# Kernel tuning notes

Hardware: AMD Instinct MI355X
Metric: run time of the kernel (lower is better)

The kernel has to match this reference:

```python
import jax, jax.numpy as jnp
import numpy as np

B, S, D, E, K = 4, 4096, 1024, 8, 2
H = 2 * D  # expert hidden dim


def setup_inputs() -> dict:
    key = jax.random.key(0)
    ks = jax.random.split(key, 7)
    scale = 0.02
    return {
        "x": jax.random.normal(ks[0], (B, S, D), dtype=jnp.float32),
        "router_w": jax.random.normal(ks[1], (D, E), dtype=jnp.float32) * scale,
        "router_b": jnp.zeros((E,), dtype=jnp.float32),
        "w1": jax.random.normal(ks[2], (E, D, H), dtype=jnp.float32) * scale,
        "b1": jnp.zeros((E, H), dtype=jnp.float32),
        "w2": jax.random.normal(ks[3], (E, H, D), dtype=jnp.float32) * scale,
        "b2": jnp.zeros((E, D), dtype=jnp.float32),
    }


def reference(x, router_w, router_b, w1, b1, w2, b2):
    # Router: softmax over experts, then top-k and renormalize
    logits = jnp.einsum("bsd,de->bse", x, router_w) + router_b
    probs = jax.nn.softmax(logits, axis=-1)
    top_p, top_i = jax.lax.top_k(probs, K)             # [B,S,K]
    top_p = top_p / jnp.sum(top_p, axis=-1, keepdims=True)

    out = jnp.zeros_like(x)
    for e in range(E):
        # gate weight for expert e per token (0 if not routed)
        gate = jnp.sum(top_p * (top_i == e), axis=-1)  # [B,S]
        h = jax.nn.relu(jnp.einsum("bsd,dh->bsh", x, w1[e]) + b1[e])
        y = jnp.einsum("bsh,hd->bsd", h, w2[e]) + b2[e]
        out = out + y * gate[..., None]
    return out
```

## Files before the change

kernel.cpp:

```cpp
#include <hip/hip_runtime.h>
#include <cstdio>
#include <cstdint>

#define N_TOK 16384
#define DIM   1024
#define NEXP  8
#define HID   2048
#define BK    64

typedef __attribute__((ext_vector_type(8))) short bf16x8;
typedef __attribute__((ext_vector_type(4))) float f32x4;

__device__ inline ushort f2bf(float f) {
  uint32_t u = __float_as_uint(f);
  uint32_t r = (u + 0x7fffu + ((u >> 16) & 1u)) >> 16;
  return (ushort)r;
}
__device__ inline float bf2f(ushort u) { return __uint_as_float(((uint32_t)u) << 16); }

__device__ __forceinline__ void gload_lds16(const void* g, void* l) {
  __builtin_amdgcn_global_load_lds((const __attribute__((address_space(1))) void*)g,
                                   (__attribute__((address_space(3))) void*)l, 16, 0, 0);
}

#define WAITV0() asm volatile("s_waitcnt vmcnt(0)" ::: "memory")
#define PBAR()  do { __builtin_amdgcn_s_barrier(); __builtin_amdgcn_sched_barrier(0); } while (0)

__global__ __launch_bounds__(256) void router_kernel(
    const float* __restrict__ x, const float* __restrict__ rw,
    const float* __restrict__ rb, int* __restrict__ blkcnt,
    int* __restrict__ tok_e, float* __restrict__ tok_g,
    ushort* __restrict__ xb) {
  __shared__ float wT[NEXP][DIM];
  __shared__ int hist[NEXP];
  if (threadIdx.x < NEXP) hist[threadIdx.x] = 0;
  for (int i = threadIdx.x; i < NEXP * DIM; i += 256) {
    int d = i >> 3, e = i & 7;
    wT[e][d] = rw[i];
  }
  __syncthreads();
  int wave = threadIdx.x >> 6, lane = threadIdx.x & 63;
  int t0 = blockIdx.x * 16 + wave * 4;
#pragma unroll
  for (int it = 0; it < 4; ++it) {
    int t = t0 + it;
    const float* xr = x + (size_t)t * DIM;
    float acc[NEXP];
#pragma unroll
    for (int e = 0; e < NEXP; ++e) acc[e] = 0.f;
#pragma unroll
    for (int j = 0; j < DIM / 64; ++j) {
      int d = lane + j * 64;
      float xv = xr[d];
#pragma unroll
      for (int e = 0; e < NEXP; ++e) acc[e] += xv * wT[e][d];
    }
    float lg[NEXP];
#pragma unroll
    for (int e = 0; e < NEXP; ++e) {
      float v = acc[e];
      for (int o = 32; o > 0; o >>= 1) v += __shfl_xor(v, o);
      lg[e] = v + rb[e];
    }
    int i0 = 0; float m0 = lg[0];
#pragma unroll
    for (int e = 1; e < NEXP; ++e) if (lg[e] > m0) { m0 = lg[e]; i0 = e; }
    int i1 = -1; float m1 = -3.4e38f;
#pragma unroll
    for (int e = 0; e < NEXP; ++e) if (e != i0 && lg[e] > m1) { m1 = lg[e]; i1 = e; }
    float g0 = 1.f / (1.f + expf(m1 - m0));
    float g1 = 1.f - g0;
    if (lane == 0) {
      tok_e[2 * t] = i0; tok_e[2 * t + 1] = i1;
      tok_g[2 * t] = g0; tok_g[2 * t + 1] = g1;
      atomicAdd(&hist[i0], 1); atomicAdd(&hist[i1], 1);
    }
  }
  {
    const float* xs = x + (size_t)blockIdx.x * 16 * DIM;
    ushort* xd = xb + (size_t)blockIdx.x * 16 * DIM;
    for (int i = threadIdx.x; i < 16 * DIM / 4; i += 256) {
      float4 v = *(const float4*)(xs + i * 4);
      ushort4 u = { f2bf(v.x), f2bf(v.y), f2bf(v.z), f2bf(v.w) };
      *(ushort4*)(xd + i * 4) = u;
    }
  }
  __syncthreads();
  if (threadIdx.x < NEXP) blkcnt[blockIdx.x * NEXP + threadIdx.x] = hist[threadIdx.x];
}

__global__ __launch_bounds__(512) void scan_kernel(const int* __restrict__ blkcnt,
                                                   int* __restrict__ blkbase,
                                                   int* __restrict__ offs) {
  __shared__ int s[64][8];
  __shared__ int chunkoff[64][8];
  __shared__ int offsh[8];
  int tid = threadIdx.x;
  int e = tid & 7, chunk = tid >> 3;
  int b0 = chunk * 16;
  int csum = 0;
#pragma unroll
  for (int b = 0; b < 16; ++b) csum += blkcnt[(b0 + b) * 8 + e];
  s[chunk][e] = csum;
  __syncthreads();
  int wave = tid >> 6, lane = tid & 63;
  int v = s[lane][wave];
  for (int o = 1; o < 64; o <<= 1) {
    int u = __shfl_up(v, o);
    if (lane >= o) v += u;
  }
  if (lane == 63) offsh[wave] = v;
  chunkoff[lane][wave] = v - s[lane][wave];
  __syncthreads();
  if (tid < 9) {
    int oe = 0;
    for (int j = 0; j < tid && j < 8; ++j) oe += offsh[j];
    offs[tid] = oe;
  }
  int oe2 = 0;
#pragma unroll
  for (int j = 0; j < 8; ++j) oe2 += (j < e) ? offsh[j] : 0;
  int base = oe2 + chunkoff[chunk][e];
  for (int b = 0; b < 16; ++b) {
    int idx = (b0 + b) * 8 + e;
    int c = blkcnt[idx];
    blkbase[idx] = base;
    base += c;
  }
}

__global__ __launch_bounds__(64) void gather_kernel(
    const int* __restrict__ tok_e, const float* __restrict__ tok_g,
    const int* __restrict__ blkbase, int* __restrict__ slot_token,
    float* __restrict__ slot_gate) {
  __shared__ int lcnt[NEXP];
  int tid = threadIdx.x, blk = blockIdx.x;
  if (tid < NEXP) lcnt[tid] = blkbase[blk * NEXP + tid];
  __syncthreads();
  if (tid < 32) {
    int t = blk * 16 + (tid >> 1);
    int k = tid & 1;
    int e = tok_e[2 * t + k];
    int s = atomicAdd(&lcnt[e], 1);
    slot_token[s] = t | (k << 16);
    slot_gate[s] = tok_g[2 * t + k];
  }
}

template <int R, int C>
__global__ __launch_bounds__(256) void transpose_cvt(const float* __restrict__ src,
                                                     ushort* __restrict__ dst) {
  __shared__ float tile[64][65];
  int e = blockIdx.z;
  const float* s = src + (size_t)e * R * C;
  ushort* d = dst + (size_t)e * R * C;
  int r0 = blockIdx.y * 64, c0 = blockIdx.x * 64;
#pragma unroll
  for (int i = 0; i < 16; ++i) {
    int idx = i * 256 + threadIdx.x;
    int r = idx >> 6, c = idx & 63;
    tile[r][c] = s[(size_t)(r0 + r) * C + c0 + c];
  }
  __syncthreads();
#pragma unroll
  for (int i = 0; i < 16; ++i) {
    int idx = i * 256 + threadIdx.x;
    int orow = idx >> 6, oc = idx & 63;
    d[(size_t)(c0 + orow) * R + r0 + oc] = f2bf(tile[oc][orow]);
  }
}


__global__ __launch_bounds__(512, 1) void gemm1_kernel(
    const ushort* __restrict__ xb, const ushort* __restrict__ w1T,
    const float* __restrict__ b1, const int* __restrict__ offs,
    const int* __restrict__ slot_token, ushort* __restrict__ h) {
  int flat = blockIdx.x;
  int swz = (flat & 7) * 512 + (flat >> 3);
  int e = swz >> 9;
  int rem = swz & 511;
  int mt = rem >> 3;
  int nt = rem & 7;
  int off = offs[e];
  int cn = offs[e + 1] - off;
  if (mt * 256 >= cn) return;

  __shared__ __align__(16) ushort AB[2 * 2 * 16384];
  __shared__ int toks[256];
  int tid = threadIdx.x;
  if (tid < 256) {
    int r = mt * 256 + tid;
    toks[tid] = slot_token[off + (r < cn ? r : 0)] & 0xffff;
  }
  __syncthreads();
  int wave = tid >> 6, lane = tid & 63;
  int wm = (wave >> 2) * 128, wn = (wave & 3) * 64;

  const ushort* Bsrc = w1T + (size_t)e * HID * DIM + (size_t)(nt * 256) * DIM;
  int colsw = (((lane & 7) ^ (lane >> 3))) * 8;
  const ushort* agp[4];
  const ushort* bgp[4];
  int ldso[4];
#pragma unroll
  for (int g = 0; g < 4; ++g) {
    int row = g * 64 + wave * 8 + (lane >> 3);
    agp[g] = xb + (size_t)toks[row] * DIM + colsw;
    bgp[g] = Bsrc + (size_t)row * DIM + colsw;
    ldso[g] = (g * 64 + wave * 8) * BK;
  }
  f32x4 acc[8][4];
#pragma unroll
  for (int i = 0; i < 8; ++i)
#pragma unroll
    for (int j = 0; j < 4; ++j) acc[i][j] = (f32x4){0.f, 0.f, 0.f, 0.f};

  int rowl = lane & 15;
  int ko0 = ((((lane >> 4) + 0)) ^ (lane & 7)) * 16 + rowl * 128;
  int ko1 = ((((lane >> 4) + 4)) ^ (lane & 7)) * 16 + rowl * 128;

  auto stage = [&](int buf) {
    ushort* lb = &AB[buf * 32768];
#pragma unroll
    for (int g = 0; g < 4; ++g) {
      gload_lds16(agp[g], lb + ldso[g]);
      gload_lds16(bgp[g], lb + 16384 + ldso[g]);
      agp[g] += BK; bgp[g] += BK;
    }
  };
  auto compute = [&](int buf) {
    const char* base = (const char*)AB + buf * 65536;
    const char* bbase = base + 32768;
    bf16x8 a[8], b[4];
#pragma unroll
    for (int mi = 0; mi < 8; ++mi) a[mi] = *(const bf16x8*)(base + (wm + mi * 16) * 128 + ko0);
#pragma unroll
    for (int ni = 0; ni < 4; ++ni) b[ni] = *(const bf16x8*)(bbase + (wn + ni * 16) * 128 + ko0);
#pragma unroll
    for (int mi = 0; mi < 8; ++mi)
#pragma unroll
      for (int ni = 0; ni < 4; ++ni)
        acc[mi][ni] = __builtin_amdgcn_mfma_f32_16x16x32_bf16(a[mi], b[ni], acc[mi][ni], 0, 0, 0);
#pragma unroll
    for (int mi = 0; mi < 8; ++mi) a[mi] = *(const bf16x8*)(base + (wm + mi * 16) * 128 + ko1);
#pragma unroll
    for (int ni = 0; ni < 4; ++ni) b[ni] = *(const bf16x8*)(bbase + (wn + ni * 16) * 128 + ko1);
#pragma unroll
    for (int mi = 0; mi < 8; ++mi)
#pragma unroll
      for (int ni = 0; ni < 4; ++ni)
        acc[mi][ni] = __builtin_amdgcn_mfma_f32_16x16x32_bf16(a[mi], b[ni], acc[mi][ni], 0, 0, 0);
  };

  const int NT = DIM / BK;
  stage(0); WAITV0(); PBAR();
  for (int kt = 0; kt < NT - 2; kt += 2) {
    stage(1); compute(0); WAITV0(); PBAR();
    stage(0); compute(1); WAITV0(); PBAR();
  }
  stage(1); compute(0); WAITV0(); PBAR();
  compute(1);

  __syncthreads();
  char* Cb = (char*)AB;
  int ln = lane & 15, lg4 = (lane >> 4) * 4;
#pragma unroll
  for (int ni = 0; ni < 4; ++ni) {
    int coll = wn + ni * 16 + ln;
    float bias = b1[(size_t)e * HID + nt * 256 + coll];
#pragma unroll
    for (int mi = 0; mi < 8; ++mi) {
#pragma unroll
      for (int rg = 0; rg < 4; ++rg) {
        int row = wm + mi * 16 + lg4 + rg;
        float v = fmaxf(acc[mi][ni][rg] + bias, 0.f);
        int slot = (coll >> 3) ^ (row & 7);
        *(ushort*)(Cb + row * 512 + slot * 16 + (coll & 7) * 2) = f2bf(v);
      }
    }
  }
  __syncthreads();
#pragma unroll
  for (int rr = 0; rr < 16; ++rr) {
    int row = rr * 16 + (tid >> 5);
    int scol = tid & 31;
    int4 v = *(const int4*)(Cb + row * 512 + ((scol ^ (row & 7)) << 4));
    int r = mt * 256 + row;
    if (r < cn)
      *(int4*)(h + (size_t)(off + r) * HID + nt * 256 + scol * 8) = v;
  }
}

__global__ __launch_bounds__(512, 1) void gemm2_kernel(
    const ushort* __restrict__ h, const ushort* __restrict__ w2T,
    const float* __restrict__ b2, const int* __restrict__ offs,
    const int* __restrict__ slot_token, const float* __restrict__ slot_gate,
    ushort* __restrict__ y) {
  int flat = blockIdx.x;
  int swz = (flat & 7) * 256 + (flat >> 3);
  int e = swz >> 8;
  int rem = swz & 255;
  int mt = rem >> 2;
  int nt = rem & 3;
  int off = offs[e];
  int cn = offs[e + 1] - off;
  if (mt * 256 >= cn) return;

  __shared__ __align__(16) ushort AB[2 * 2 * 16384];
  __shared__ int yrows[256];
  __shared__ float gts[256];
  int tid = threadIdx.x;
  if (tid < 256) {
    int r = mt * 256 + tid;
    int s = off + (r < cn ? r : 0);
    int tk = slot_token[s];
    yrows[tid] = ((tk & 0xffff) << 1) | (tk >> 16);
    gts[tid] = slot_gate[s];
  }
  __syncthreads();
  int wave = tid >> 6, lane = tid & 63;
  int wm = (wave >> 2) * 128, wn = (wave & 3) * 64;

  const ushort* Bsrc = w2T + (size_t)e * DIM * HID + (size_t)(nt * 256) * HID;
  int colsw = (((lane & 7) ^ (lane >> 3))) * 8;
  const ushort* agp[4];
  const ushort* bgp[4];
  int ldso[4];
#pragma unroll
  for (int g = 0; g < 4; ++g) {
    int row = g * 64 + wave * 8 + (lane >> 3);
    int rr = mt * 256 + row; rr = rr < cn ? rr : 0;
    agp[g] = h + (size_t)(off + rr) * HID + colsw;
    bgp[g] = Bsrc + (size_t)row * HID + colsw;
    ldso[g] = (g * 64 + wave * 8) * BK;
  }
  f32x4 acc[8][4];
#pragma unroll
  for (int i = 0; i < 8; ++i)
#pragma unroll
    for (int j = 0; j < 4; ++j) acc[i][j] = (f32x4){0.f, 0.f, 0.f, 0.f};

  int rowl = lane & 15;
  int ko0 = ((((lane >> 4) + 0)) ^ (lane & 7)) * 16 + rowl * 128;
  int ko1 = ((((lane >> 4) + 4)) ^ (lane & 7)) * 16 + rowl * 128;

  auto stage = [&](int buf) {
    ushort* lb = &AB[buf * 32768];
#pragma unroll
    for (int g = 0; g < 4; ++g) {
      gload_lds16(agp[g], lb + ldso[g]);
      gload_lds16(bgp[g], lb + 16384 + ldso[g]);
      agp[g] += BK; bgp[g] += BK;
    }
  };
  auto compute = [&](int buf) {
    const char* base = (const char*)AB + buf * 65536;
    const char* bbase = base + 32768;
    bf16x8 a[8], b[4];
#pragma unroll
    for (int mi = 0; mi < 8; ++mi) a[mi] = *(const bf16x8*)(base + (wm + mi * 16) * 128 + ko0);
#pragma unroll
    for (int ni = 0; ni < 4; ++ni) b[ni] = *(const bf16x8*)(bbase + (wn + ni * 16) * 128 + ko0);
#pragma unroll
    for (int mi = 0; mi < 8; ++mi)
#pragma unroll
      for (int ni = 0; ni < 4; ++ni)
        acc[mi][ni] = __builtin_amdgcn_mfma_f32_16x16x32_bf16(a[mi], b[ni], acc[mi][ni], 0, 0, 0);
#pragma unroll
    for (int mi = 0; mi < 8; ++mi) a[mi] = *(const bf16x8*)(base + (wm + mi * 16) * 128 + ko1);
#pragma unroll
    for (int ni = 0; ni < 4; ++ni) b[ni] = *(const bf16x8*)(bbase + (wn + ni * 16) * 128 + ko1);
#pragma unroll
    for (int mi = 0; mi < 8; ++mi)
#pragma unroll
      for (int ni = 0; ni < 4; ++ni)
        acc[mi][ni] = __builtin_amdgcn_mfma_f32_16x16x32_bf16(a[mi], b[ni], acc[mi][ni], 0, 0, 0);
  };

  const int NT = HID / BK;
  stage(0); WAITV0(); PBAR();
  for (int kt = 0; kt < NT - 2; kt += 2) {
    stage(1); compute(0); WAITV0(); PBAR();
    stage(0); compute(1); WAITV0(); PBAR();
  }
  stage(1); compute(0); WAITV0(); PBAR();
  compute(1);

  __syncthreads();
  char* Cb = (char*)AB;
  int ln = lane & 15, lg4 = (lane >> 4) * 4;
#pragma unroll
  for (int ni = 0; ni < 4; ++ni) {
    int coll = wn + ni * 16 + ln;
    float bias = b2[(size_t)e * DIM + nt * 256 + coll];
#pragma unroll
    for (int mi = 0; mi < 8; ++mi) {
#pragma unroll
      for (int rg = 0; rg < 4; ++rg) {
        int row = wm + mi * 16 + lg4 + rg;
        float v = gts[row] * (acc[mi][ni][rg] + bias);
        int slot = (coll >> 3) ^ (row & 7);
        *(ushort*)(Cb + row * 512 + slot * 16 + (coll & 7) * 2) = f2bf(v);
      }
    }
  }
  __syncthreads();
#pragma unroll
  for (int rr = 0; rr < 16; ++rr) {
    int row = rr * 16 + (tid >> 5);
    int scol = tid & 31;
    int4 v = *(const int4*)(Cb + row * 512 + ((scol ^ (row & 7)) << 4));
    int r = mt * 256 + row;
    if (r < cn)
      *(int4*)(y + (size_t)yrows[row] * DIM + nt * 256 + scol * 8) = v;
  }
}

__global__ __launch_bounds__(256) void combine_kernel(float* __restrict__ out) {
  int t = blockIdx.x;
  int d = threadIdx.x;
  const ushort* y = (const ushort*)out;
  ushort4 a = *(const ushort4*)(y + (size_t)(2 * t) * DIM + 4 * d);
  ushort4 b = *(const ushort4*)(y + (size_t)(2 * t + 1) * DIM + 4 * d);
  float4 r;
  r.x = bf2f(a.x) + bf2f(b.x);
  r.y = bf2f(a.y) + bf2f(b.y);
  r.z = bf2f(a.z) + bf2f(b.z);
  r.w = bf2f(a.w) + bf2f(b.w);
  __syncthreads();
  *(float4*)(out + (size_t)t * DIM + 4 * d) = r;
}

extern "C" void kernel_launch(void* const* d_in, const int* in_sizes, int n_in,
                              void* d_out, int out_size, void* d_ws, size_t ws_size,
                              hipStream_t stream) {
  const float* x  = (const float*)d_in[0];
  const float* rw = (const float*)d_in[1];
  const float* rb = (const float*)d_in[2];
  const float* w1 = (const float*)d_in[3];
  const float* b1 = (const float*)d_in[4];
  const float* w2 = (const float*)d_in[5];
  const float* b2 = (const float*)d_in[6];
  float* out = (float*)d_out;
  char* ws = (char*)d_ws;

  const size_t o_ctrl = 0;
  const size_t o_toke = 256;
  const size_t o_tokg = o_toke + 131072;
  const size_t o_stok = o_tokg + 131072;
  const size_t o_sgat = o_stok + 131072;
  const size_t o_xb   = o_sgat + 131072;
  const size_t o_w1T  = o_xb + (size_t)N_TOK * DIM * 2;
  const size_t o_h    = o_w1T + (size_t)NEXP * HID * DIM * 2;
  const size_t required = o_h + (size_t)N_TOK * 2 * HID * 2;
  if (ws_size < required) {
    fprintf(stderr, "kernel_launch: ws too small: have %zu need %zu\n", ws_size, required);
    return;
  }
  int* offs       = (int*)(ws + o_ctrl);
  int* tok_e      = (int*)(ws + o_toke);
  float* tok_g    = (float*)(ws + o_tokg);
  int* slot_token = (int*)(ws + o_stok);
  float* slot_gate= (float*)(ws + o_sgat);
  ushort* xb      = (ushort*)(ws + o_xb);
  ushort* w2T     = (ushort*)(ws + o_xb);
  ushort* w1T     = (ushort*)(ws + o_w1T);
  ushort* hbuf    = (ushort*)(ws + o_h);
  int* blkcnt     = (int*)(ws + o_h);
  int* blkbase    = blkcnt + 1024 * NEXP;

  hipMemsetAsync(d_out, 0, (size_t)out_size * 4, stream);
  hipMemsetAsync(ws + o_ctrl, 0, 64, stream);

  router_kernel<<<N_TOK / 16, 256, 0, stream>>>(x, rw, rb, blkcnt, tok_e, tok_g, xb);
  scan_kernel<<<1, 512, 0, stream>>>(blkcnt, blkbase, offs);
  gather_kernel<<<N_TOK / 16, 64, 0, stream>>>(tok_e, tok_g, blkbase, slot_token, slot_gate);

  transpose_cvt<DIM, HID><<<dim3(HID / 64, DIM / 64, NEXP), 256, 0, stream>>>(w1, w1T);

  gemm1_kernel<<<8 * 64 * NEXP, 512, 0, stream>>>(xb, w1T, b1, offs, slot_token, hbuf);

  transpose_cvt<HID, DIM><<<dim3(DIM / 64, HID / 64, NEXP), 256, 0, stream>>>(w2, w2T);

  gemm2_kernel<<<4 * 64 * NEXP, 512, 0, stream>>>(hbuf, w2T, b2, offs, slot_token, slot_gate,
                                                  (ushort*)d_out);
  combine_kernel<<<N_TOK, 256, 0, stream>>>(out);
}
```

Measured before the change: 454.2 us.

## Deepen GEMM pipelines to four LDS stages with BK=32 and drop memsets

Both expert GEMM kernels switch from a double-buffered BK=64 loop that waits for all loads each step to a four-buffer BK=32 ring. Three stages are kept in flight, and partial vmcnt waits let global-to-LDS loads overlap MFMA work instead of draining the queue at every step. The LDS swizzle and the per-lane load mapping are reworked for the 64-byte rows. Separately, the two hipMemsetAsync calls on the output and control area are removed. That saves launches but is only correct if nothing depends on the zeroing, which is a risk for the offset/control counters.

Result: faster. 431.5 us (-5.0%).

```diff
diff --git a/kernel.cpp b/kernel.cpp
--- a/kernel.cpp
+++ b/kernel.cpp
@@ -6,7 +6,7 @@
 #define DIM   1024
 #define NEXP  8
 #define HID   2048
-#define BK    64
+#define BK    32
 
 typedef __attribute__((ext_vector_type(8))) short bf16x8;
 typedef __attribute__((ext_vector_type(4))) float f32x4;
@@ -23,7 +23,7 @@
                                    (__attribute__((address_space(3))) void*)l, 16, 0, 0);
 }
 
-#define WAITV0() asm volatile("s_waitcnt vmcnt(0)" ::: "memory")
+#define WAITV(N) asm volatile("s_waitcnt vmcnt(" #N ")" ::: "memory")
 #define PBAR()  do { __builtin_amdgcn_s_barrier(); __builtin_amdgcn_sched_barrier(0); } while (0)
 
 __global__ __launch_bounds__(256) void router_kernel(
@@ -185,7 +185,7 @@
   int cn = offs[e + 1] - off;
   if (mt * 256 >= cn) return;
 
-  __shared__ __align__(16) ushort AB[2 * 2 * 16384];
+  __shared__ __align__(16) ushort AB[4 * 16384];
   __shared__ int toks[256];
   int tid = threadIdx.x;
   if (tid < 256) {
@@ -197,53 +197,41 @@
   int wm = (wave >> 2) * 128, wn = (wave & 3) * 64;
 
   const ushort* Bsrc = w1T + (size_t)e * HID * DIM + (size_t)(nt * 256) * DIM;
-  int colsw = (((lane & 7) ^ (lane >> 3))) * 8;
-  const ushort* agp[4];
-  const ushort* bgp[4];
-  int ldso[4];
-#pragma unroll
-  for (int g = 0; g < 4; ++g) {
-    int row = g * 64 + wave * 8 + (lane >> 3);
-    agp[g] = xb + (size_t)toks[row] * DIM + colsw;
-    bgp[g] = Bsrc + (size_t)row * DIM + colsw;
-    ldso[g] = (g * 64 + wave * 8) * BK;
-  }
+  int colsw = ((lane & 3) ^ ((lane >> 3) & 3)) * 8;
+  int r0 = wave * 16 + (lane >> 2);
+  const ushort* ag0 = xb + (size_t)toks[r0] * DIM + colsw;
+  const ushort* ag1 = xb + (size_t)toks[128 + r0] * DIM + colsw;
+  const ushort* bg0 = Bsrc + (size_t)r0 * DIM + colsw;
+  const ushort* bg1 = Bsrc + (size_t)(128 + r0) * DIM + colsw;
+  int ldsA0 = (wave * 16) * BK;
+  int ldsA1 = (128 + wave * 16) * BK;
+  int ldsB0 = 8192 + ldsA0;
+  int ldsB1 = 8192 + ldsA1;
+
   f32x4 acc[8][4];
 #pragma unroll
   for (int i = 0; i < 8; ++i)
 #pragma unroll
     for (int j = 0; j < 4; ++j) acc[i][j] = (f32x4){0.f, 0.f, 0.f, 0.f};
 
-  int rowl = lane & 15;
-  int ko0 = ((((lane >> 4) + 0)) ^ (lane & 7)) * 16 + rowl * 128;
-  int ko1 = ((((lane >> 4) + 4)) ^ (lane & 7)) * 16 + rowl * 128;
+  int rdo = (lane & 15) * 64 + ((((lane >> 4) & 3) << 4) ^ ((((lane & 15) >> 1) & 3) << 4));
 
   auto stage = [&](int buf) {
-    ushort* lb = &AB[buf * 32768];
-#pragma unroll
-    for (int g = 0; g < 4; ++g) {
-      gload_lds16(agp[g], lb + ldso[g]);
-      gload_lds16(bgp[g], lb + 16384 + ldso[g]);
-      agp[g] += BK; bgp[g] += BK;
-    }
+    ushort* lb = &AB[buf * 16384];
+    gload_lds16(ag0, lb + ldsA0); ag0 += BK;
+    gload_lds16(ag1, lb + ldsA1); ag1 += BK;
+    gload_lds16(bg0, lb + ldsB0); bg0 += BK;
+    gload_lds16(bg1, lb + ldsB1); bg1 += BK;
   };
   auto compute = [&](int buf) {
-    const char* base = (const char*)AB + buf * 65536;
-    const char* bbase = base + 32768;
+    const char* base = (const char*)AB + (size_t)buf * 32768;
     bf16x8 a[8], b[4];
 #pragma unroll
-    for (int mi = 0; mi < 8; ++mi) a[mi] = *(const bf16x8*)(base + (wm + mi * 16) * 128 + ko0);
-#pragma unroll
-    for (int ni = 0; ni < 4; ++ni) b[ni] = *(const bf16x8*)(bbase + (wn + ni * 16) * 128 + ko0);
-#pragma unroll
     for (int mi = 0; mi < 8; ++mi)
-#pragma unroll
-      for (int ni = 0; ni < 4; ++ni)
-        acc[mi][ni] = __builtin_amdgcn_mfma_f32_16x16x32_bf16(a[mi], b[ni], acc[mi][ni], 0, 0, 0);
-#pragma unroll
-    for (int mi = 0; mi < 8; ++mi) a[mi] = *(const bf16x8*)(base + (wm + mi * 16) * 128 + ko1);
-#pragma unroll
-    for (int ni = 0; ni < 4; ++ni) b[ni] = *(const bf16x8*)(bbase + (wn + ni * 16) * 128 + ko1);
+      a[mi] = *(const bf16x8*)(base + (wm + mi * 16) * 64 + rdo);
+#pragma unroll
+    for (int ni = 0; ni < 4; ++ni)
+      b[ni] = *(const bf16x8*)(base + 16384 + (wn + ni * 16) * 64 + rdo);
 #pragma unroll
     for (int mi = 0; mi < 8; ++mi)
 #pragma unroll
@@ -251,14 +239,18 @@
         acc[mi][ni] = __builtin_amdgcn_mfma_f32_16x16x32_bf16(a[mi], b[ni], acc[mi][ni], 0, 0, 0);
   };
 
-  const int NT = DIM / BK;
-  stage(0); WAITV0(); PBAR();
-  for (int kt = 0; kt < NT - 2; kt += 2) {
-    stage(1); compute(0); WAITV0(); PBAR();
-    stage(0); compute(1); WAITV0(); PBAR();
-  }
-  stage(1); compute(0); WAITV0(); PBAR();
-  compute(1);
+  const int T = DIM / BK;
+  stage(0); stage(1); stage(2);
+  for (int t4 = 0; t4 < T - 4; t4 += 4) {
+    WAITV(8); PBAR(); stage(3); compute(0);
+    WAITV(8); PBAR(); stage(0); compute(1);
+    WAITV(8); PBAR(); stage(1); compute(2);
+    WAITV(8); PBAR(); stage(2); compute(3);
+  }
+  WAITV(8); PBAR(); stage(3); compute(0);
+  WAITV(8); PBAR(); compute(1);
+  WAITV(4); PBAR(); compute(2);
+  WAITV(0); PBAR(); compute(3);
 
   __syncthreads();
   char* Cb = (char*)AB;
@@ -305,7 +297,7 @@
   int cn = offs[e + 1] - off;
   if (mt * 256 >= cn) return;
 
-  __shared__ __align__(16) ushort AB[2 * 2 * 16384];
+  __shared__ __align__(16) ushort AB[4 * 16384];
   __shared__ int yrows[256];
   __shared__ float gts[256];
   int tid = threadIdx.x;
@@ -321,54 +313,43 @@
   int wm = (wave >> 2) * 128, wn = (wave & 3) * 64;
 
   const ushort* Bsrc = w2T + (size_t)e * DIM * HID + (size_t)(nt * 256) * HID;
-  int colsw = (((lane & 7) ^ (lane >> 3))) * 8;
-  const ushort* agp[4];
-  const ushort* bgp[4];
-  int ldso[4];
-#pragma unroll
-  for (int g = 0; g < 4; ++g) {
-    int row = g * 64 + wave * 8 + (lane >> 3);
-    int rr = mt * 256 + row; rr = rr < cn ? rr : 0;
-    agp[g] = h + (size_t)(off + rr) * HID + colsw;
-    bgp[g] = Bsrc + (size_t)row * HID + colsw;
-    ldso[g] = (g * 64 + wave * 8) * BK;
-  }
+  int colsw = ((lane & 3) ^ ((lane >> 3) & 3)) * 8;
+  int r0 = wave * 16 + (lane >> 2);
+  int ra0 = mt * 256 + r0;       ra0 = ra0 < cn ? ra0 : 0;
+  int ra1 = mt * 256 + 128 + r0; ra1 = ra1 < cn ? ra1 : 0;
+  const ushort* ag0 = h + (size_t)(off + ra0) * HID + colsw;
+  const ushort* ag1 = h + (size_t)(off + ra1) * HID + colsw;
+  const ushort* bg0 = Bsrc + (size_t)r0 * HID + colsw;
+  const ushort* bg1 = Bsrc + (size_t)(128 + r0) * HID + colsw;
+  int ldsA0 = (wave * 16) * BK;
+  int ldsA1 = (128 + wave * 16) * BK;
+  int ldsB0 = 8192 + ldsA0;
+  int ldsB1 = 8192 + ldsA1;
+
   f32x4 acc[8][4];
 #pragma unroll
   for (int i = 0; i < 8; ++i)
 #pragma unroll
     for (int j = 0; j < 4; ++j) acc[i][j] = (f32x4){0.f, 0.f, 0.f, 0.f};
 
-  int rowl = lane & 15;
-  int ko0 = ((((lane >> 4) + 0)) ^ (lane & 7)) * 16 + rowl * 128;
-  int ko1 = ((((lane >> 4) + 4)) ^ (lane & 7)) * 16 + rowl * 128;
+  int rdo = (lane & 15) * 64 + ((((lane >> 4) & 3) << 4) ^ ((((lane & 15) >> 1) & 3) << 4));
 
   auto stage = [&](int buf) {
-    ushort* lb = &AB[buf * 32768];
-#pragma unroll
-    for (int g = 0; g < 4; ++g) {
-      gload_lds16(agp[g], lb + ldso[g]);
-      gload_lds16(bgp[g], lb + 16384 + ldso[g]);
-      agp[g] += BK; bgp[g] += BK;
-    }
+    ushort* lb = &AB[buf * 16384];
+    gload_lds16(ag0, lb + ldsA0); ag0 += BK;
+    gload_lds16(ag1, lb + ldsA1); ag1 += BK;
+    gload_lds16(bg0, lb + ldsB0); bg0 += BK;
+    gload_lds16(bg1, lb + ldsB1); bg1 += BK;
   };
   auto compute = [&](int buf) {
-    const char* base = (const char*)AB + buf * 65536;
-    const char* bbase = base + 32768;
+    const char* base = (const char*)AB + (size_t)buf * 32768;
     bf16x8 a[8], b[4];
 #pragma unroll
-    for (int mi = 0; mi < 8; ++mi) a[mi] = *(const bf16x8*)(base + (wm + mi * 16) * 128 + ko0);
-#pragma unroll
-    for (int ni = 0; ni < 4; ++ni) b[ni] = *(const bf16x8*)(bbase + (wn + ni * 16) * 128 + ko0);
-#pragma unroll
     for (int mi = 0; mi < 8; ++mi)
-#pragma unroll
-      for (int ni = 0; ni < 4; ++ni)
-        acc[mi][ni] = __builtin_amdgcn_mfma_f32_16x16x32_bf16(a[mi], b[ni], acc[mi][ni], 0, 0, 0);
-#pragma unroll
-    for (int mi = 0; mi < 8; ++mi) a[mi] = *(const bf16x8*)(base + (wm + mi * 16) * 128 + ko1);
-#pragma unroll
-    for (int ni = 0; ni < 4; ++ni) b[ni] = *(const bf16x8*)(bbase + (wn + ni * 16) * 128 + ko1);
+      a[mi] = *(const bf16x8*)(base + (wm + mi * 16) * 64 + rdo);
+#pragma unroll
+    for (int ni = 0; ni < 4; ++ni)
+      b[ni] = *(const bf16x8*)(base + 16384 + (wn + ni * 16) * 64 + rdo);
 #pragma unroll
     for (int mi = 0; mi < 8; ++mi)
 #pragma unroll
@@ -376,14 +357,18 @@
         acc[mi][ni] = __builtin_amdgcn_mfma_f32_16x16x32_bf16(a[mi], b[ni], acc[mi][ni], 0, 0, 0);
   };
 
-  const int NT = HID / BK;
-  stage(0); WAITV0(); PBAR();
-  for (int kt = 0; kt < NT - 2; kt += 2) {
-    stage(1); compute(0); WAITV0(); PBAR();
-    stage(0); compute(1); WAITV0(); PBAR();
-  }
-  stage(1); compute(0); WAITV0(); PBAR();
-  compute(1);
+  const int T = HID / BK;
+  stage(0); stage(1); stage(2);
+  for (int t4 = 0; t4 < T - 4; t4 += 4) {
+    WAITV(8); PBAR(); stage(3); compute(0);
+    WAITV(8); PBAR(); stage(0); compute(1);
+    WAITV(8); PBAR(); stage(1); compute(2);
+    WAITV(8); PBAR(); stage(2); compute(3);
+  }
+  WAITV(8); PBAR(); stage(3); compute(0);
+  WAITV(8); PBAR(); compute(1);
+  WAITV(4); PBAR(); compute(2);
+  WAITV(0); PBAR(); compute(3);
 
   __syncthreads();
   char* Cb = (char*)AB;
@@ -468,8 +453,6 @@
   int* blkcnt     = (int*)(ws + o_h);
   int* blkbase    = blkcnt + 1024 * NEXP;
 
-  hipMemsetAsync(d_out, 0, (size_t)out_size * 4, stream);
-  hipMemsetAsync(ws + o_ctrl, 0, 64, stream);
 
   router_kernel<<<N_TOK / 16, 256, 0, stream>>>(x, rw, rb, blkcnt, tok_e, tok_g, xb);
   scan_kernel<<<1, 512, 0, stream>>>(blkcnt, blkbase, offs);
```
